# Kernel optimization log

Measured on AMD Instinct MI355X. Metric: run time of the kernel, lower is better.

Reference implementation:

```python
import jax, jax.numpy as jnp
import numpy as np
from jax import lax

HIDDEN = 512
EPS = 1e-5


def _conv(x, w):
    # NCHW conv, 3x3, SAME padding, no bias (padding = kernel_size // 2 == 1)
    return lax.conv_general_dilated(
        x, w, window_strides=(1, 1), padding='SAME',
        dimension_numbers=('NCHW', 'OIHW', 'NCHW'))


def setup_inputs() -> dict:
    key = jax.random.key(0)
    ks = jax.random.split(key, 5)
    N, C, H, W = 32, HIDDEN, 32, 32
    fan = C * 9
    std = float(1.0 / np.sqrt(fan))
    return {
        'x': jax.random.normal(ks[0], (N, C, H, W), jnp.float32),
        'w_q': jax.random.normal(ks[1], (C, C, 3, 3), jnp.float32) * std,
        'w_k': jax.random.normal(ks[2], (C, C, 3, 3), jnp.float32) * std,
        'w_v': jax.random.normal(ks[3], (C, C, 3, 3), jnp.float32) * std,
        'w_o': jax.random.normal(ks[4], (C, C, 3, 3), jnp.float32) * std,
        'gamma': jnp.ones((C,), jnp.float32),
        'beta': jnp.zeros((C,), jnp.float32),
    }


def reference(x, w_q, w_k, w_v, w_o, gamma, beta):
    C = x.shape[1]
    q = _conv(x, w_q)  # [N,C,H,W]
    k = _conv(x, w_k)
    v = _conv(x, w_v)
    # (query.unsqueeze(1) * key.unsqueeze(0)).sum(2) == channel contraction
    att = jnp.einsum('ichw,jchw->ijhw', q, k) / jnp.sqrt(jnp.asarray(C, x.dtype))
    att = jax.nn.softmax(att, axis=1)  # softmax over key instances
    virt = jnp.einsum('ijhw,jchw->ichw', att, v)  # [N,C,H,W]
    # GroupNorm(1, C): normalize over (C,H,W) per instance, per-channel affine
    mean = jnp.mean(virt, axis=(1, 2, 3), keepdims=True)
    var = jnp.var(virt, axis=(1, 2, 3), keepdims=True)
    virt = (virt - mean) * lax.rsqrt(var + EPS)
    virt = virt * gamma[None, :, None, None] + beta[None, :, None, None]
    virt = jax.nn.relu(virt)
    virt = _conv(virt, w_o)
    # Dropout(0.2) is identity in eval mode
    return x + virt
```

## Files before the change

### kernel.cpp

```cpp
#include <hip/hip_runtime.h>

namespace {

constexpr int kN  = 32;
constexpr int kC  = 512;
constexpr int kH  = 32;
constexpr int kW  = 32;
constexpr int kHW = kH * kW;

constexpr int PCH   = 36992;
constexpr size_t WTF_ELEMS = (size_t)9 * kC * kC;
constexpr size_t XH_ELEMS  = (size_t)kN * 16 * PCH;
constexpr size_t QKV_ELEMS = (size_t)kN * kHW * kC;

using bf16x8 = __attribute__((ext_vector_type(8))) short;
using bf16x4 = __attribute__((ext_vector_type(4))) short;
using f32x4  = __attribute__((ext_vector_type(4))) float;

__device__ __forceinline__ float bf2f(short s) {
  unsigned u = ((unsigned)(unsigned short)s) << 16;
  return __builtin_bit_cast(float, u);
}
__device__ __forceinline__ short f2bf(float f) {
  unsigned u = __builtin_bit_cast(unsigned, f);
  u += 0x7FFFu + ((u >> 16) & 1u);
  return (short)(u >> 16);
}
__device__ __forceinline__ void gload_lds16(const void* g, void* l) {
  __builtin_amdgcn_global_load_lds(
      (const __attribute__((address_space(1))) void*)g,
      (__attribute__((address_space(3))) void*)l, 16, 0, 0);
}

__global__ __launch_bounds__(256) void wtf_pack_kernel(
    const float* __restrict__ w, short* __restrict__ wtf) {
  __shared__ float tile[32][289];
  const int co0 = blockIdx.x * 32;
  const int ci0 = blockIdx.y * 32;
  for (int idx = threadIdx.x; idx < 32 * 288; idx += 256) {
    int c = idx % 288, r = idx / 288;
    tile[r][c] = w[(size_t)(co0 + r) * (kC * 9) + (size_t)ci0 * 9 + c];
  }
  __syncthreads();
  const int kkb  = ci0 >> 5;
  const int nnG0 = co0 >> 4;
  for (int g = threadIdx.x; g < 9 * 2 * 64; g += 256) {
    int laneg = g & 63;
    int nnL   = (g >> 6) & 1;
    int t     = g >> 7;
    int hi    = laneg >> 4;
    int coL   = nnL * 16 + (laneg & 15);
    bf16x8 pk;
#pragma unroll
    for (int j = 0; j < 8; ++j) pk[j] = f2bf(tile[coL][(hi * 8 + j) * 9 + t]);
    *(bf16x8*)&wtf[(((size_t)t * 16 + kkb) * 32 + nnG0 + nnL) * 512 + laneg * 8] = pk;
  }
}

__global__ __launch_bounds__(256) void x2xh_kernel(
    const float* __restrict__ x, short* __restrict__ xh) {
  __shared__ float tile[32][33];
  const int ch = blockIdx.x;
  const int h  = blockIdx.y;
  const int n  = blockIdx.z;
  const int w0 = threadIdx.x & 31;
  const int c0 = threadIdx.x >> 5;
#pragma unroll
  for (int pass = 0; pass < 4; ++pass) {
    int cir = pass * 8 + c0;
    tile[w0][cir] = x[(((size_t)n * kC + ch * 32 + cir) * kH + h) * kW + w0];
  }
  __syncthreads();
  const int wv = threadIdx.x >> 3;
  const int g4 = (threadIdx.x & 7) * 4;
  bf16x4 pk;
#pragma unroll
  for (int j = 0; j < 4; ++j) pk[j] = f2bf(tile[wv][g4 + j]);
  *(bf16x4*)&xh[(((size_t)n * 16 + ch) * 1156 + (size_t)(h + 1) * 34 + (wv + 1)) * 32 + g4] = pk;
}

__global__ __launch_bounds__(256, 2) void conv_qkv_kernel(
    const short* __restrict__ xin,
    const short* __restrict__ wtq, const short* __restrict__ wtk,
    const short* __restrict__ wtv,
    short* __restrict__ outq, short* __restrict__ outk,
    short* __restrict__ outv) {
  __shared__ __align__(16) short As[3][8192];
  const int tid  = threadIdx.x;
  const int lane = tid & 63;
  const int l15  = lane & 15, lhi = lane >> 4;
  const int w    = tid >> 6;
  const int wbase = tid & 192;

  const int xcd = blockIdx.x & 7;
  const int m   = blockIdx.x >> 3;
  const int co0 = (m >> 5) * 64;
  const int spt = m & 7;
  const int n   = xcd * 4 + ((m >> 3) & 3);
  const int h0  = spt * 4;
  const int sp0 = spt * 128;

  const short* srcA = xin + (size_t)n * (16 * PCH) + (size_t)h0 * (34 * 32);
  const size_t boff = ((size_t)(co0 >> 4) + w) * 512 + lane * 8;
  const short* bp[3] = {wtq + boff, wtk + boff, wtv + boff};

  f32x4 acc[3][8];
#pragma unroll
  for (int c = 0; c < 3; ++c)
#pragma unroll
    for (int mf = 0; mf < 8; ++mf)
#pragma unroll
      for (int r = 0; r < 4; ++r) acc[c][mf][r] = 0.f;

#define STAGE_A(kk, buf)                                                      \
  {                                                                           \
    const short* gA = srcA + (size_t)(kk) * PCH;                              \
    _Pragma("unroll") for (int pass = 0; pass < 4; ++pass)                    \
        gload_lds16(gA + (size_t)(pass * 256 + tid) * 8,                      \
                    &As[buf][(pass * 256 + wbase) * 8]);                      \
  }

  STAGE_A(0, 0);
  STAGE_A(1, 1);
  bf16x8 cur[3], nxt[3];
#pragma unroll
  for (int j = 0; j < 3; ++j)
    cur[j] = *(const bf16x8*)&bp[j][0];

  int ab = 0;
  int sb = 2;
  for (int kk = 0; kk < 16; ++kk) {
    asm volatile("s_waitcnt vmcnt(7)" ::: "memory");
    __builtin_amdgcn_s_barrier();
#pragma unroll
    for (int t = 0; t < 9; ++t) {
      {
        const int nt  = (t < 8) ? (t + 1) : 0;
        const int nkk = (t < 8) ? kk : kk + 1;
        const size_t bo = (size_t)(nt * 16 + nkk) * 16384;
#pragma unroll
        for (int j = 0; j < 3; ++j)
          nxt[j] = *(const bf16x8*)&bp[j][bo];
      }
      if (t == 1 && kk < 14) STAGE_A(kk + 2, sb);
      const int dy = t / 3, dx = t % 3;
      bf16x8 a[8];
#pragma unroll
      for (int mf = 0; mf < 8; ++mf) {
        const int pb = ((mf >> 1) + dy) * 34 + (mf & 1) * 16 + l15 + dx;
        a[mf] = *(const bf16x8*)&As[ab][pb * 32 + lhi * 8];
      }
      __builtin_amdgcn_s_setprio(1);
#pragma unroll
      for (int c = 0; c < 3; ++c)
#pragma unroll
        for (int mf = 0; mf < 8; ++mf)
          acc[c][mf] = __builtin_amdgcn_mfma_f32_16x16x32_bf16(
              a[mf], cur[c], acc[c][mf], 0, 0, 0);
      __builtin_amdgcn_s_setprio(0);
#pragma unroll
      for (int j = 0; j < 3; ++j) cur[j] = nxt[j];
    }
    ab = (ab == 2) ? 0 : ab + 1;
    sb = (sb == 2) ? 0 : sb + 1;
  }
#undef STAGE_A

  short* outs[3] = {outq, outk, outv};
#pragma unroll
  for (int c = 0; c < 3; ++c) {
    short* out = outs[c];
#pragma unroll
    for (int mf = 0; mf < 8; ++mf)
#pragma unroll
      for (int r = 0; r < 4; ++r) {
        size_t off = ((size_t)n * kHW + sp0 + mf * 16 + lhi * 4 + r) * kC
                     + co0 + w * 16 + l15;
        out[off] = f2bf(acc[c][mf][r]);
      }
  }
}

__global__ __launch_bounds__(256, 3) void conv_o_kernel(
    const short* __restrict__ xin, const short* __restrict__ wtf,
    const float* __restrict__ xres, float* __restrict__ out) {
  __shared__ __align__(16) short As[3][8192];
  const int tid  = threadIdx.x;
  const int lane = tid & 63;
  const int l15  = lane & 15, lhi = lane >> 4;
  const int wv   = tid >> 6;
  const int wm   = wv >> 1, wn = wv & 1;
  const int wbase = tid & 192;

  const int xcd = blockIdx.x & 7;
  const int m   = blockIdx.x >> 3;
  const int co0 = (m >> 5) * 128;
  const int spt = m & 7;
  const int n   = xcd * 4 + ((m >> 3) & 3);
  const int h0  = spt * 4;
  const int sp0 = spt * 128;

  const short* srcA = xin + (size_t)n * (16 * PCH) + (size_t)h0 * (34 * 32);
  const short* bptr = wtf + ((size_t)(co0 >> 4) + wn * 4) * 512 + lane * 8;

  f32x4 acc[4][4];
#pragma unroll
  for (int mf = 0; mf < 4; ++mf)
#pragma unroll
    for (int nf = 0; nf < 4; ++nf)
#pragma unroll
      for (int r = 0; r < 4; ++r) acc[mf][nf][r] = 0.f;

#define STAGE_A(kk, buf)                                                      \
  {                                                                           \
    const short* gA = srcA + (size_t)(kk) * PCH;                              \
    _Pragma("unroll") for (int pass = 0; pass < 4; ++pass)                    \
        gload_lds16(gA + (size_t)(pass * 256 + tid) * 8,                      \
                    &As[buf][(pass * 256 + wbase) * 8]);                      \
  }

  STAGE_A(0, 0);
  STAGE_A(1, 1);
  bf16x8 cur[4], nxt[4];
#pragma unroll
  for (int j = 0; j < 4; ++j)
    cur[j] = *(const bf16x8*)&bptr[(size_t)j * 512];

  int ab = 0, sb = 2;
  for (int kk = 0; kk < 16; ++kk) {
    asm volatile("s_waitcnt vmcnt(8)" ::: "memory");
    __builtin_amdgcn_s_barrier();
#pragma unroll
    for (int t = 0; t < 9; ++t) {
      {
        const int nt  = (t < 8) ? (t + 1) : 0;
        const int nkk = (t < 8) ? kk : kk + 1;
        const size_t bo = (size_t)(nt * 16 + nkk) * 16384;
#pragma unroll
        for (int j = 0; j < 4; ++j)
          nxt[j] = *(const bf16x8*)&bptr[bo + (size_t)j * 512];
      }
      if (t == 1 && kk < 14) STAGE_A(kk + 2, sb);
      const int dy = t / 3, dx = t % 3;
      bf16x8 a[4];
#pragma unroll
      for (int mf = 0; mf < 4; ++mf) {
        const int pb = (wm * 2 + (mf >> 1) + dy) * 34 + (mf & 1) * 16 + l15 + dx;
        a[mf] = *(const bf16x8*)&As[ab][pb * 32 + lhi * 8];
      }
      __builtin_amdgcn_s_setprio(1);
#pragma unroll
      for (int mf = 0; mf < 4; ++mf)
#pragma unroll
        for (int nf = 0; nf < 4; ++nf)
          acc[mf][nf] = __builtin_amdgcn_mfma_f32_16x16x32_bf16(
              a[mf], cur[nf], acc[mf][nf], 0, 0, 0);
      __builtin_amdgcn_s_setprio(0);
#pragma unroll
      for (int j = 0; j < 4; ++j) cur[j] = nxt[j];
    }
    ab = (ab == 2) ? 0 : ab + 1;
    sb = (sb == 2) ? 0 : sb + 1;
  }
#undef STAGE_A

  float* T = (float*)&As[0][0];
#pragma unroll
  for (int nf = 0; nf < 4; ++nf) {
    __syncthreads();
    const int coL = wn * 16 + l15;
#pragma unroll
    for (int mf = 0; mf < 4; ++mf)
#pragma unroll
      for (int r = 0; r < 4; ++r)
        T[coL * 129 + wm * 64 + mf * 16 + lhi * 4 + r] = acc[mf][nf][r];
    __syncthreads();
#pragma unroll
    for (int it = 0; it < 16; ++it) {
      int idx = it * 256 + tid;
      int c = idx >> 7, sp = idx & 127;
      int co = co0 + (c >> 4) * 64 + nf * 16 + (c & 15);
      size_t off = ((size_t)n * kC + co) * kHW + sp0 + sp;
      out[off] = T[c * 129 + sp] + xres[off];
    }
  }
}

__global__ __launch_bounds__(256) void attn_mfma_kernel(
    const short* q, const short* __restrict__ k,
    const short* __restrict__ v, short* virt) {
  __shared__ __align__(16) short Qs[32 * 72];
  __shared__ __align__(16) short Ks[32 * 72];
  __shared__ __align__(16) float Ps[32 * 36];
  __shared__ __align__(16) short Vt[64 * 40];
  const int p    = blockIdx.x;
  const int tid  = threadIdx.x;
  const int lane = tid & 63;
  const int l15  = lane & 15, lhi = lane >> 4;
  const int w    = tid >> 6;
  const int iq   = w >> 1, jq = w & 1;

  f32x4 accS = {0.f, 0.f, 0.f, 0.f};
  const int si = tid >> 3;
  const int sc = (tid & 7) * 8;
  for (int c0 = 0; c0 < kC; c0 += 64) {
    __syncthreads();
    {
      size_t g = ((size_t)si * kHW + p) * kC + c0 + sc;
      *(bf16x8*)&Qs[si * 72 + sc] = *(const bf16x8*)&q[g];
      *(bf16x8*)&Ks[si * 72 + sc] = *(const bf16x8*)&k[g];
    }
    __syncthreads();
#pragma unroll
    for (int cs = 0; cs < 2; ++cs) {
      bf16x8 aq = *(const bf16x8*)&Qs[(iq * 16 + l15) * 72 + cs * 32 + lhi * 8];
      bf16x8 bk = *(const bf16x8*)&Ks[(jq * 16 + l15) * 72 + cs * 32 + lhi * 8];
      accS = __builtin_amdgcn_mfma_f32_16x16x32_bf16(aq, bk, accS, 0, 0, 0);
    }
  }
  __syncthreads();
  constexpr float scale = 0.044194173824159216f;
#pragma unroll
  for (int r = 0; r < 4; ++r)
    Ps[(iq * 16 + lhi * 4 + r) * 36 + jq * 16 + l15] = accS[r] * scale;
  __syncthreads();

  {
    const int i  = tid >> 3;
    const int j0 = (tid & 7) * 4;
    float a0 = Ps[i * 36 + j0], a1 = Ps[i * 36 + j0 + 1];
    float a2 = Ps[i * 36 + j0 + 2], a3 = Ps[i * 36 + j0 + 3];
    float mx = fmaxf(fmaxf(a0, a1), fmaxf(a2, a3));
    for (int off = 1; off < 8; off <<= 1) mx = fmaxf(mx, __shfl_xor(mx, off));
    float e0 = __expf(a0 - mx), e1 = __expf(a1 - mx);
    float e2 = __expf(a2 - mx), e3 = __expf(a3 - mx);
    float s = e0 + e1 + e2 + e3;
    for (int off = 1; off < 8; off <<= 1) s += __shfl_xor(s, off);
    const float inv = 1.f / s;
    Ps[i * 36 + j0]     = e0 * inv;
    Ps[i * 36 + j0 + 1] = e1 * inv;
    Ps[i * 36 + j0 + 2] = e2 * inv;
    Ps[i * 36 + j0 + 3] = e3 * inv;
  }
  __syncthreads();

  bf16x8 ap[2];
#pragma unroll
  for (int it = 0; it < 2; ++it) {
    const float* pr = &Ps[(it * 16 + l15) * 36 + lhi * 8];
    float4 lo = *(const float4*)pr;
    float4 hi4 = *(const float4*)(pr + 4);
    ap[it][0] = f2bf(lo.x);  ap[it][1] = f2bf(lo.y);
    ap[it][2] = f2bf(lo.z);  ap[it][3] = f2bf(lo.w);
    ap[it][4] = f2bf(hi4.x); ap[it][5] = f2bf(hi4.y);
    ap[it][6] = f2bf(hi4.z); ap[it][7] = f2bf(hi4.w);
  }

  const f32x4 zacc = {0.f, 0.f, 0.f, 0.f};
  for (int c0 = 0; c0 < kC; c0 += 64) {
    __syncthreads();
    {
      const int j = tid >> 3, c8g = tid & 7;
      bf16x8 vvv = *(const bf16x8*)&v[((size_t)j * kHW + p) * kC + c0 + c8g * 8];
#pragma unroll
      for (int jj = 0; jj < 8; ++jj) {
        int c = c8g * 8 + jj;
        int byte = (c * 80 + j * 2) ^ (((c >> 3) & 7) << 4);
        *(short*)((char*)Vt + byte) = vvv[jj];
      }
    }
    __syncthreads();
    {
      const int c = w * 16 + l15;
      const int byte = (c * 80 + lhi * 16) ^ (((c >> 3) & 7) << 4);
      bf16x8 bv = *(const bf16x8*)((const char*)Vt + byte);
#pragma unroll
      for (int it = 0; it < 2; ++it) {
        f32x4 o = __builtin_amdgcn_mfma_f32_16x16x32_bf16(ap[it], bv, zacc, 0, 0, 0);
#pragma unroll
        for (int r = 0; r < 4; ++r)
          virt[((size_t)(it * 16 + lhi * 4 + r) * kHW + p) * kC + c0 + w * 16 + l15] =
              f2bf(o[r]);
      }
    }
  }
}

__global__ __launch_bounds__(256) void gn_part_kernel(
    const short* __restrict__ virt, float* __restrict__ part) {
  const int i   = blockIdx.x >> 3;
  const int seg = blockIdx.x & 7;
  const short* src = virt + (size_t)i * kHW * kC + (size_t)seg * (kHW * kC / 8);
  float s = 0.f, sq = 0.f;
  for (int idx = threadIdx.x; idx < kHW * kC / 8 / 8; idx += 256) {
    bf16x8 vv = *(const bf16x8*)&src[(size_t)idx * 8];
#pragma unroll
    for (int jj = 0; jj < 8; ++jj) {
      float f = bf2f(vv[jj]);
      s += f;
      sq = fmaf(f, f, sq);
    }
  }
  __shared__ float rs[4], rq[4];
  for (int off = 1; off < 64; off <<= 1) {
    s += __shfl_xor(s, off);
    sq += __shfl_xor(sq, off);
  }
  const int lane = threadIdx.x & 63;
  const int wid = threadIdx.x >> 6;
  if (lane == 0) { rs[wid] = s; rq[wid] = sq; }
  __syncthreads();
  if (threadIdx.x == 0) {
    part[blockIdx.x]       = rs[0] + rs[1] + rs[2] + rs[3];
    part[256 + blockIdx.x] = rq[0] + rq[1] + rq[2] + rq[3];
  }
}

__global__ __launch_bounds__(64) void gn_final_kernel(
    const float* __restrict__ part, float* __restrict__ stats) {
  if (threadIdx.x < 32) {
    float s = 0.f, sq = 0.f;
#pragma unroll
    for (int kq = 0; kq < 8; ++kq) {
      s  += part[threadIdx.x * 8 + kq];
      sq += part[256 + threadIdx.x * 8 + kq];
    }
    constexpr float invn = 1.f / ((float)kHW * kC);
    float mean = s * invn;
    float var = sq * invn - mean * mean;
    stats[threadIdx.x] = mean;
    stats[32 + threadIdx.x] = rsqrtf(var + 1e-5f);
  }
}

__global__ __launch_bounds__(256) void gn_apply_kernel(
    const short* __restrict__ virt, const float* __restrict__ stats,
    const float* __restrict__ gamma, const float* __restrict__ beta,
    short* __restrict__ vh) {
  const size_t g = (size_t)blockIdx.x * 256 + threadIdx.x;
  const int i    = (int)(g >> 16);
  const int rest = (int)(g & 65535);
  const int p    = rest >> 6;
  const int c8g  = rest & 63;
  const int ci   = c8g * 8;
  const float mean = stats[i];
  const float rstd = stats[32 + i];
  bf16x8 vv = *(const bf16x8*)&virt[((size_t)i * kHW + p) * kC + ci];
  const float4 ga = ((const float4*)gamma)[c8g * 2];
  const float4 gb = ((const float4*)gamma)[c8g * 2 + 1];
  const float4 ba = ((const float4*)beta)[c8g * 2];
  const float4 bb = ((const float4*)beta)[c8g * 2 + 1];
  const float gv[8] = {ga.x, ga.y, ga.z, ga.w, gb.x, gb.y, gb.z, gb.w};
  const float bv[8] = {ba.x, ba.y, ba.z, ba.w, bb.x, bb.y, bb.z, bb.w};
  bf16x8 o;
#pragma unroll
  for (int jj = 0; jj < 8; ++jj) {
    float f = (bf2f(vv[jj]) - mean) * rstd;
    f = fmaxf(fmaf(f, gv[jj], bv[jj]), 0.f);
    o[jj] = f2bf(f);
  }
  const size_t dst =
      (((size_t)i * 16 + (ci >> 5)) * 1156 + (size_t)((p >> 5) + 1) * 34 + (p & 31) + 1) * 32
      + (ci & 31);
  *(bf16x8*)&vh[dst] = o;
}

}

extern "C" void kernel_launch(void* const* d_in, const int* in_sizes, int n_in,
                              void* d_out, int out_size, void* d_ws,
                              size_t ws_size, hipStream_t stream) {
  const float* x     = (const float*)d_in[0];
  const float* w_q   = (const float*)d_in[1];
  const float* w_k   = (const float*)d_in[2];
  const float* w_v   = (const float*)d_in[3];
  const float* w_o   = (const float*)d_in[4];
  const float* gamma = (const float*)d_in[5];
  const float* beta  = (const float*)d_in[6];

  short* ws    = (short*)d_ws;
  short* wtf_q = ws;
  short* wtf_k = wtf_q + WTF_ELEMS;
  short* wtf_v = wtf_k + WTF_ELEMS;
  short* wtf_o = wtf_v + WTF_ELEMS;
  short* xh    = wtf_o + WTF_ELEMS;
  short* vh    = xh + XH_ELEMS;
  short* qb    = vh + XH_ELEMS;
  short* kb    = qb + QKV_ELEMS;
  short* vb    = kb + QKV_ELEMS;
  float* stats = (float*)(vb + QKV_ELEMS);
  float* part  = stats + 64;
  short* virt  = qb;
  hipMemsetAsync(xh, 0, (size_t)2 * XH_ELEMS * sizeof(short), stream);

  dim3 wg(16, 16);
  wtf_pack_kernel<<<wg, 256, 0, stream>>>(w_q, wtf_q);
  wtf_pack_kernel<<<wg, 256, 0, stream>>>(w_k, wtf_k);
  wtf_pack_kernel<<<wg, 256, 0, stream>>>(w_v, wtf_v);
  wtf_pack_kernel<<<wg, 256, 0, stream>>>(w_o, wtf_o);

  x2xh_kernel<<<dim3(16, 32, 32), 256, 0, stream>>>(x, xh);

  conv_qkv_kernel<<<2048, 256, 0, stream>>>(xh, wtf_q, wtf_k, wtf_v,
                                            qb, kb, vb);

  attn_mfma_kernel<<<kHW, 256, 0, stream>>>(qb, kb, vb, virt);

  gn_part_kernel<<<256, 256, 0, stream>>>(virt, part);
  gn_final_kernel<<<1, 64, 0, stream>>>(part, stats);
  gn_apply_kernel<<<(int)(QKV_ELEMS / 8 / 256), 256, 0, stream>>>(
      virt, stats, gamma, beta, vh);

  conv_o_kernel<<<1024, 256, 0, stream>>>(vh, wtf_o, x, (float*)d_out);
}
```

Baseline: 565.4 us.

## Fuse GroupNorm statistics into attention kernel and batch weight packing

Computes the per-instance GroupNorm sum and sum of squares inside the attention kernel from the rounded bf16 outputs. The partial sums are reduced with shuffles and shared memory, then added into a global buffer with atomics, which removes the separate pass that re-read the 32MB virt tensor. The four weight-pack launches are also merged into one launch using a z-dimension grid. This adds 64 atomics per block over 1024 blocks, an extra memset, and an order-dependent float summation.

```diff
diff --git a/kernel.cpp b/kernel.cpp
--- a/kernel.cpp
+++ b/kernel.cpp
@@ -33,7 +33,14 @@
 }
 
 __global__ __launch_bounds__(256) void wtf_pack_kernel(
-    const float* __restrict__ w, short* __restrict__ wtf) {
+    const float* __restrict__ wq, const float* __restrict__ wk,
+    const float* __restrict__ wv, const float* __restrict__ wo,
+    short* __restrict__ oq, short* __restrict__ ok,
+    short* __restrict__ ov, short* __restrict__ oo) {
+  const float* wsrc[4] = {wq, wk, wv, wo};
+  short* wdst[4] = {oq, ok, ov, oo};
+  const float* w = wsrc[blockIdx.z];
+  short* wtf = wdst[blockIdx.z];
   __shared__ float tile[32][289];
   const int co0 = blockIdx.x * 32;
   const int ci0 = blockIdx.y * 32;
@@ -288,7 +295,7 @@
 
 __global__ __launch_bounds__(256) void attn_mfma_kernel(
     const short* q, const short* __restrict__ k,
-    const short* __restrict__ v, short* virt) {
+    const short* __restrict__ v, short* virt, float* __restrict__ gsum) {
   __shared__ __align__(16) short Qs[32 * 72];
   __shared__ __align__(16) short Ks[32 * 72];
   __shared__ __align__(16) float Ps[32 * 36];
@@ -355,6 +362,11 @@
     ap[it][4] = f2bf(hi4.x); ap[it][5] = f2bf(hi4.y);
     ap[it][6] = f2bf(hi4.z); ap[it][7] = f2bf(hi4.w);
   }
+  __syncthreads();
+
+  float gs[8], gq2[8];
+#pragma unroll
+  for (int idx = 0; idx < 8; ++idx) { gs[idx] = 0.f; gq2[idx] = 0.f; }
 
   const f32x4 zacc = {0.f, 0.f, 0.f, 0.f};
   for (int c0 = 0; c0 < kC; c0 += 64) {
@@ -378,56 +390,53 @@
       for (int it = 0; it < 2; ++it) {
         f32x4 o = __builtin_amdgcn_mfma_f32_16x16x32_bf16(ap[it], bv, zacc, 0, 0, 0);
 #pragma unroll
-        for (int r = 0; r < 4; ++r)
-          virt[((size_t)(it * 16 + lhi * 4 + r) * kHW + p) * kC + c0 + w * 16 + l15] =
-              f2bf(o[r]);
-      }
-    }
-  }
-}
-
-__global__ __launch_bounds__(256) void gn_part_kernel(
-    const short* __restrict__ virt, float* __restrict__ part) {
-  const int i   = blockIdx.x >> 3;
-  const int seg = blockIdx.x & 7;
-  const short* src = virt + (size_t)i * kHW * kC + (size_t)seg * (kHW * kC / 8);
-  float s = 0.f, sq = 0.f;
-  for (int idx = threadIdx.x; idx < kHW * kC / 8 / 8; idx += 256) {
-    bf16x8 vv = *(const bf16x8*)&src[(size_t)idx * 8];
-#pragma unroll
-    for (int jj = 0; jj < 8; ++jj) {
-      float f = bf2f(vv[jj]);
-      s += f;
-      sq = fmaf(f, f, sq);
-    }
-  }
-  __shared__ float rs[4], rq[4];
-  for (int off = 1; off < 64; off <<= 1) {
-    s += __shfl_xor(s, off);
-    sq += __shfl_xor(sq, off);
-  }
-  const int lane = threadIdx.x & 63;
-  const int wid = threadIdx.x >> 6;
-  if (lane == 0) { rs[wid] = s; rq[wid] = sq; }
-  __syncthreads();
-  if (threadIdx.x == 0) {
-    part[blockIdx.x]       = rs[0] + rs[1] + rs[2] + rs[3];
-    part[256 + blockIdx.x] = rq[0] + rq[1] + rq[2] + rq[3];
+        for (int r = 0; r < 4; ++r) {
+          short ob = f2bf(o[r]);
+          virt[((size_t)(it * 16 + lhi * 4 + r) * kHW + p) * kC + c0 + w * 16 + l15] = ob;
+          float fv = bf2f(ob);
+          gs[it * 4 + r] += fv;
+          gq2[it * 4 + r] = fmaf(fv, fv, gq2[it * 4 + r]);
+        }
+      }
+    }
+  }
+
+#pragma unroll
+  for (int idx = 0; idx < 8; ++idx)
+    for (int off = 1; off < 16; off <<= 1) {
+      gs[idx]  += __shfl_xor(gs[idx], off);
+      gq2[idx] += __shfl_xor(gq2[idx], off);
+    }
+  __syncthreads();
+  float* SS = Ps;
+  if (l15 == 0) {
+#pragma unroll
+    for (int idx = 0; idx < 8; ++idx) {
+      int it = idx >> 2, r = idx & 3;
+      int i = it * 16 + lhi * 4 + r;
+      SS[(w * 32 + i) * 2]     = gs[idx];
+      SS[(w * 32 + i) * 2 + 1] = gq2[idx];
+    }
+  }
+  __syncthreads();
+  if (tid < 32) {
+    float s = 0.f, q2 = 0.f;
+#pragma unroll
+    for (int ww = 0; ww < 4; ++ww) {
+      s  += SS[(ww * 32 + tid) * 2];
+      q2 += SS[(ww * 32 + tid) * 2 + 1];
+    }
+    atomicAdd(&gsum[tid], s);
+    atomicAdd(&gsum[32 + tid], q2);
   }
 }
 
 __global__ __launch_bounds__(64) void gn_final_kernel(
-    const float* __restrict__ part, float* __restrict__ stats) {
+    const float* __restrict__ gsum, float* __restrict__ stats) {
   if (threadIdx.x < 32) {
-    float s = 0.f, sq = 0.f;
-#pragma unroll
-    for (int kq = 0; kq < 8; ++kq) {
-      s  += part[threadIdx.x * 8 + kq];
-      sq += part[256 + threadIdx.x * 8 + kq];
-    }
     constexpr float invn = 1.f / ((float)kHW * kC);
-    float mean = s * invn;
-    float var = sq * invn - mean * mean;
+    float mean = gsum[threadIdx.x] * invn;
+    float var = gsum[32 + threadIdx.x] * invn - mean * mean;
     stats[threadIdx.x] = mean;
     stats[32 + threadIdx.x] = rsqrtf(var + 1e-5f);
   }
@@ -489,25 +498,22 @@
   short* kb    = qb + QKV_ELEMS;
   short* vb    = kb + QKV_ELEMS;
   float* stats = (float*)(vb + QKV_ELEMS);
-  float* part  = stats + 64;
+  float* gsum  = stats + 64;
   short* virt  = qb;
   hipMemsetAsync(xh, 0, (size_t)2 * XH_ELEMS * sizeof(short), stream);
-
-  dim3 wg(16, 16);
-  wtf_pack_kernel<<<wg, 256, 0, stream>>>(w_q, wtf_q);
-  wtf_pack_kernel<<<wg, 256, 0, stream>>>(w_k, wtf_k);
-  wtf_pack_kernel<<<wg, 256, 0, stream>>>(w_v, wtf_v);
-  wtf_pack_kernel<<<wg, 256, 0, stream>>>(w_o, wtf_o);
+  hipMemsetAsync(gsum, 0, 64 * sizeof(float), stream);
+
+  wtf_pack_kernel<<<dim3(16, 16, 4), 256, 0, stream>>>(
+      w_q, w_k, w_v, w_o, wtf_q, wtf_k, wtf_v, wtf_o);
 
   x2xh_kernel<<<dim3(16, 32, 32), 256, 0, stream>>>(x, xh);
 
   conv_qkv_kernel<<<2048, 256, 0, stream>>>(xh, wtf_q, wtf_k, wtf_v,
                                             qb, kb, vb);
 
-  attn_mfma_kernel<<<kHW, 256, 0, stream>>>(qb, kb, vb, virt);
-
-  gn_part_kernel<<<256, 256, 0, stream>>>(virt, part);
-  gn_final_kernel<<<1, 64, 0, stream>>>(part, stats);
+  attn_mfma_kernel<<<kHW, 256, 0, stream>>>(qb, kb, vb, virt, gsum);
+
+  gn_final_kernel<<<1, 64, 0, stream>>>(gsum, stats);
   gn_apply_kernel<<<(int)(QKV_ELEMS / 8 / 256), 256, 0, stream>>>(
       virt, stats, gamma, beta, vh);
 
```

Result: no change. 563.6 us (-0.3%).
